# Optimization experiments

Measured on AMD Instinct MI355X. Metric: run time of the kernel, lower is better.

## Reference

```python
import jax, jax.numpy as jnp
import numpy as np

TOP_K = 32
OBS_RADIUS = 1.0
N = 4096
IN_DIM = 4


def setup_inputs() -> dict:
    key = jax.random.key(0)
    ks = jax.random.split(key, 10)
    s = 0.05
    return {
        "states": jax.random.normal(ks[0], (N, 4), jnp.float32),
        "goals": jax.random.normal(ks[1], (N, 2), jnp.float32),
        "W1": jax.random.normal(ks[2], (64, IN_DIM + 1), jnp.float32) * s,
        "b1": jnp.zeros((64,), jnp.float32),
        "W2": jax.random.normal(ks[3], (128, 64), jnp.float32) * s,
        "b2": jnp.zeros((128,), jnp.float32),
        "Wd1": jax.random.normal(ks[4], (64, 132), jnp.float32) * s,
        "bd1": jnp.zeros((64,), jnp.float32),
        "Wd2": jax.random.normal(ks[5], (128, 64), jnp.float32) * s,
        "bd2": jnp.zeros((128,), jnp.float32),
        "Wd3": jax.random.normal(ks[6], (64, 128), jnp.float32) * s,
        "bd3": jnp.zeros((64,), jnp.float32),
        "Wd4": jax.random.normal(ks[7], (4, 64), jnp.float32) * s,
        "bd4": jnp.zeros((4,), jnp.float32),
    }


def reference(states, goals, W1, b1, W2, b2, Wd1, bd1, Wd2, bd2, Wd3, bd3, Wd4, bd4):
    n = states.shape[0]
    dt = states.dtype
    # pairwise relative states + one-hot self indicator -> [N, N, 5]
    x = states[:, None, :] - states[None, :, :]
    x = jnp.concatenate([x, jnp.eye(n, dtype=dt)[:, :, None]], axis=2)
    # remove_distant_agents: keep TOP_K nearest neighbors by planar distance
    d = jnp.sqrt(jnp.sum(x[:, :, :2] ** 2, axis=2) + 1e-4)  # [N, N]
    _, idx = jax.lax.top_k(-d, TOP_K)                        # [N, K]
    xk = jnp.take_along_axis(x, idx[:, :, None], axis=1)     # [N, K, 5]
    # observation-radius mask (torch reshape [N,K,1]->[N,1,K] == transpose here)
    dist = jnp.linalg.norm(xk[:, :, :2], axis=2)             # [N, K]
    mask = (dist < OBS_RADIUS).astype(dt).reshape(n, 1, TOP_K)
    # NOTE: original uses a raw reshape [N,K,5]->[N,5,K] (not a transpose); match it
    h = xk.reshape(n, IN_DIM + 1, TOP_K)
    # pointwise (kernel-1) conv stack 5 -> 64 -> 128
    h = jax.nn.relu(jnp.einsum('oc,ncp->nop', W1, h) + b1[None, :, None])
    h = jax.nn.relu(jnp.einsum('oc,ncp->nop', W2, h) + b2[None, :, None])
    # original does torch.max(...)[1]: ARGMAX indices, promoted to float by cat
    x_local = jnp.argmax(h * mask, axis=2).astype(dt)        # [N, 128]
    rel = states[:, :2] - goals
    feat = jnp.concatenate([x_local, rel, states[:, 2:]], axis=1)  # [N, 132]
    z = jax.nn.relu(feat @ Wd1.T + bd1)
    z = jax.nn.relu(z @ Wd2.T + bd2)
    z = jax.nn.relu(z @ Wd3.T + bd3)
    z = z @ Wd4.T + bd4
    k = 2.0 * jax.nn.sigmoid(z) + 0.2                        # [N, 4] gains
    state = jnp.concatenate([rel, states[:, 2:]], axis=1)    # [N, 4]
    a_x = -(k[:, 0] * state[:, 0] + k[:, 1] * state[:, 2])
    a_y = -(k[:, 2] * state[:, 1] + k[:, 3] * state[:, 3])
    return jnp.stack([a_x, a_y], axis=1)                     # [N, 2]
```

## Files before the change

### kernel.cpp

```cpp
#include <hip/hip_runtime.h>
#include <math.h>

#define NAGENT 4096
#define TOPK 32
#define FAGB 8
#define CANDCAP 2048

__global__ __launch_bounds__(256) void topk_kernel(
    const float* __restrict__ states, int* __restrict__ idx_out)
{
    const int i = blockIdx.x;
    const int t = threadIdx.x;
    const int lane = t & 63;
    __shared__ unsigned int hist[1024];
    __shared__ unsigned int wsum[4];
    __shared__ unsigned long long cand[CANDCAP];
    __shared__ int ccount;
    __shared__ unsigned int cutB;

    #pragma unroll
    for (int u = 0; u < 4; ++u) hist[t + u * 256] = 0u;
    if (t == 0) ccount = 0;

    const float4 si = ((const float4*)states)[i];
    __syncthreads();

    unsigned int mybits[16];
    #pragma unroll
    for (int u = 0; u < 16; ++u) {
        int j = t + u * 256;
        float4 sj = ((const float4*)states)[j];
        float dx = __fsub_rn(si.x, sj.x);
        float dy = __fsub_rn(si.y, sj.y);
        float s  = __fadd_rn(__fadd_rn(__fmul_rn(dx, dx), __fmul_rn(dy, dy)), 1e-4f);
        float dv = sqrtf(s);
        mybits[u] = __float_as_uint(dv);
        unsigned int bin = (unsigned int)(dv * 256.0f);
        if (bin > 1023u) bin = 1023u;
        atomicAdd(&hist[bin], 1u);
    }
    __syncthreads();

    unsigned int h0 = hist[t * 4 + 0], h1 = hist[t * 4 + 1];
    unsigned int h2 = hist[t * 4 + 2], h3 = hist[t * 4 + 3];
    unsigned int v = h0 + h1 + h2 + h3;
    unsigned int inc = v;
    #pragma unroll
    for (int off = 1; off < 64; off <<= 1) {
        unsigned int u = __shfl_up(inc, off, 64);
        if (lane >= off) inc += u;
    }
    if (lane == 63) wsum[t >> 6] = inc;
    __syncthreads();
    unsigned int woff = 0;
    for (int w = 0; w < (t >> 6); ++w) woff += wsum[w];
    unsigned int incl = inc + woff;
    unsigned int exc  = incl - v;
    if (exc < TOPK && incl >= TOPK) {
        unsigned int cum = exc;
        unsigned int hh[4] = {h0, h1, h2, h3};
        int b = t * 4 + 3;
        #pragma unroll
        for (int q = 0; q < 4; ++q) {
            cum += hh[q];
            if (cum >= TOPK) { b = t * 4 + q; break; }
        }
        cutB = (unsigned int)b;
    }
    __syncthreads();

    const unsigned int B = cutB;
    #pragma unroll
    for (int u = 0; u < 16; ++u) {
        float dv = __uint_as_float(mybits[u]);
        unsigned int bin = (unsigned int)(dv * 256.0f);
        if (bin > 1023u) bin = 1023u;
        if (bin <= B) {
            int pos = atomicAdd(&ccount, 1);
            if (pos < CANDCAP)
                cand[pos] = ((unsigned long long)mybits[u] << 32)
                          | (unsigned int)(t + u * 256);
        }
    }
    __syncthreads();

    const int C = (ccount < CANDCAP) ? ccount : CANDCAP;
    for (int q = t; q < C; q += 256) {
        unsigned long long key = cand[q];
        int rank = 0;
        for (int r = 0; r < C; ++r) rank += (cand[r] < key) ? 1 : 0;
        if (rank < TOPK) idx_out[i * TOPK + rank] = (int)(key & 0xffffffffu);
    }
}

__global__ __launch_bounds__(256) void fused_kernel(
    const float* __restrict__ states, const float* __restrict__ goals,
    const float* __restrict__ W1,  const float* __restrict__ b1,
    const float* __restrict__ W2,  const float* __restrict__ b2,
    const float* __restrict__ Wd1, const float* __restrict__ bd1,
    const float* __restrict__ Wd2, const float* __restrict__ bd2,
    const float* __restrict__ Wd3, const float* __restrict__ bd3,
    const float* __restrict__ Wd4, const float* __restrict__ bd4,
    const int* __restrict__ idx_in, float* __restrict__ out)
{
    const int t = threadIdx.x;
    const int a = t >> 6;
    const int l = t & 63;
    const int base = blockIdx.x * FAGB;

    __shared__ __attribute__((aligned(16))) float w2a[64 * 68];
    __shared__ __attribute__((aligned(16))) float w2b[64 * 68];
    __shared__ __attribute__((aligned(16))) float w1s[320];
    __shared__ __attribute__((aligned(16))) float b1s[64];
    __shared__ __attribute__((aligned(16))) float b2s[128];
    __shared__ __attribute__((aligned(16))) float flat[4][160];
    __shared__ __attribute__((aligned(16))) float maskv[4][32];
    __shared__ __attribute__((aligned(16))) float featb[FAGB][132];
    __shared__ __attribute__((aligned(16))) float h1[4][2048];
    float* z1s = &h1[0][0];
    float* z2s = z1s + 512;
    float* z3s = z2s + 1024;
    float* kvs = z3s + 512;

    #pragma unroll
    for (int u = 0; u < 32; ++u) {
        int e = t + u * 256;
        int o = e >> 6, c = e & 63;
        float v = W2[e];
        int dst = c * 68 + ((o >> 3) << 2) + (o & 3);
        if (o & 4) w2b[dst] = v; else w2a[dst] = v;
    }
    for (int e = t; e < 320; e += 256) w1s[e] = W1[e];
    if (t < 64)  b1s[t] = b1[t];
    if (t < 128) b2s[t] = b2[t];
    __syncthreads();

    #pragma unroll
    for (int round = 0; round < 2; ++round) {
        const int g = round * 4 + a;
        const int i = base + g;

        if (l < 32) {
            int j = idx_in[i * TOPK + l];
            float4 sj  = ((const float4*)states)[j];
            float4 siv = ((const float4*)states)[i];
            float d0 = siv.x - sj.x;
            float d1 = siv.y - sj.y;
            float d2 = siv.z - sj.z;
            float d3 = siv.w - sj.w;
            flat[a][l * 5 + 0] = d0;
            flat[a][l * 5 + 1] = d1;
            flat[a][l * 5 + 2] = d2;
            flat[a][l * 5 + 3] = d3;
            flat[a][l * 5 + 4] = (j == i) ? 1.0f : 0.0f;
            float dist = sqrtf(__fadd_rn(__fmul_rn(d0, d0), __fmul_rn(d1, d1)));
            maskv[a][l] = (dist < 1.0f) ? 1.0f : 0.0f;
        } else if (l < 36) {
            int f = l - 32;
            float4 siv = ((const float4*)states)[i];
            float2 gi  = ((const float2*)goals)[i];
            float v = (f == 0) ? (siv.x - gi.x)
                    : (f == 1) ? (siv.y - gi.y)
                    : (f == 2) ? siv.z : siv.w;
            featb[g][128 + f] = v;
        }

        #pragma unroll
        for (int u = 0; u < 32; ++u) {
            int e = u * 64 + l;
            int p = e & 31, o1 = e >> 5;
            float acc = b1s[o1];
            #pragma unroll
            for (int f = 0; f < 5; ++f)
                acc += w1s[o1 * 5 + f] * flat[a][f * 32 + p];
            h1[a][o1 * 32 + p] = fmaxf(acc, 0.0f);
        }

        const int ow = l & 15;
        const int pt = l >> 4;
        float acc[8][8];
        #pragma unroll
        for (int k = 0; k < 8; ++k)
            #pragma unroll
            for (int q = 0; q < 8; ++q) acc[k][q] = 0.0f;

        for (int c4 = 0; c4 < 16; ++c4) {
            float4 wAv[4], wBv[4], hAv[4], hBv[4];
            #pragma unroll
            for (int cc = 0; cc < 4; ++cc) {
                int c = c4 * 4 + cc;
                wAv[cc] = *(const float4*)&w2a[c * 68 + ow * 4];
                wBv[cc] = *(const float4*)&w2b[c * 68 + ow * 4];
                hAv[cc] = *(const float4*)&h1[a][c * 32 + pt * 8];
                hBv[cc] = *(const float4*)&h1[a][c * 32 + pt * 8 + 4];
            }
            #pragma unroll
            for (int cc = 0; cc < 4; ++cc) {
                float wv[8] = {wAv[cc].x, wAv[cc].y, wAv[cc].z, wAv[cc].w,
                               wBv[cc].x, wBv[cc].y, wBv[cc].z, wBv[cc].w};
                float hv[8] = {hAv[cc].x, hAv[cc].y, hAv[cc].z, hAv[cc].w,
                               hBv[cc].x, hBv[cc].y, hBv[cc].z, hBv[cc].w};
                #pragma unroll
                for (int k = 0; k < 8; ++k)
                    #pragma unroll
                    for (int q = 0; q < 8; ++q)
                        acc[k][q] += wv[k] * hv[q];
            }
        }

        float4 mA = *(const float4*)&maskv[a][pt * 8];
        float4 mB = *(const float4*)&maskv[a][pt * 8 + 4];
        float mv[8] = {mA.x, mA.y, mA.z, mA.w, mB.x, mB.y, mB.z, mB.w};
        #pragma unroll
        for (int k = 0; k < 8; ++k) {
            float bb = b2s[ow * 8 + k];
            unsigned long long best = 0ull;
            #pragma unroll
            for (int q = 0; q < 8; ++q) {
                float val = fmaxf(acc[k][q] + bb, 0.0f) * mv[q];
                unsigned long long key =
                    ((unsigned long long)__float_as_uint(val) << 32)
                    | (unsigned int)(31 - (pt * 8 + q));
                if (key > best) best = key;
            }
            unsigned long long o1 = __shfl_xor(best, 16, 64); if (o1 > best) best = o1;
            unsigned long long o2 = __shfl_xor(best, 32, 64); if (o2 > best) best = o2;
            if (pt == 0) {
                int pbest = 31 - (int)(best & 63ull);
                featb[g][ow * 8 + k] = (float)pbest;
            }
        }
    }
    __syncthreads();

    const int g0 = 2 * a, g1 = 2 * a + 1;

    {
        float bb = bd1[l];
        float a0 = bb, a1 = bb;
        for (int k = 0; k < 33; ++k) {
            float4 wv = *(const float4*)&Wd1[l * 132 + 4 * k];
            float4 f0 = *(const float4*)&featb[g0][4 * k];
            float4 f1 = *(const float4*)&featb[g1][4 * k];
            a0 += wv.x * f0.x; a0 += wv.y * f0.y; a0 += wv.z * f0.z; a0 += wv.w * f0.w;
            a1 += wv.x * f1.x; a1 += wv.y * f1.y; a1 += wv.z * f1.z; a1 += wv.w * f1.w;
        }
        z1s[g0 * 64 + l] = fmaxf(a0, 0.0f);
        z1s[g1 * 64 + l] = fmaxf(a1, 0.0f);
    }

    {
        float accA0 = bd2[l], accA1 = bd2[l];
        float accB0 = bd2[l + 64], accB1 = bd2[l + 64];
        for (int k = 0; k < 16; ++k) {
            float4 wa = *(const float4*)&Wd2[l * 64 + 4 * k];
            float4 wb = *(const float4*)&Wd2[(l + 64) * 64 + 4 * k];
            float4 f0 = *(const float4*)&z1s[g0 * 64 + 4 * k];
            float4 f1 = *(const float4*)&z1s[g1 * 64 + 4 * k];
            accA0 += wa.x * f0.x; accA0 += wa.y * f0.y;
            accA0 += wa.z * f0.z; accA0 += wa.w * f0.w;
            accB0 += wb.x * f0.x; accB0 += wb.y * f0.y;
            accB0 += wb.z * f0.z; accB0 += wb.w * f0.w;
            accA1 += wa.x * f1.x; accA1 += wa.y * f1.y;
            accA1 += wa.z * f1.z; accA1 += wa.w * f1.w;
            accB1 += wb.x * f1.x; accB1 += wb.y * f1.y;
            accB1 += wb.z * f1.z; accB1 += wb.w * f1.w;
        }
        z2s[g0 * 128 + l]      = fmaxf(accA0, 0.0f);
        z2s[g0 * 128 + l + 64] = fmaxf(accB0, 0.0f);
        z2s[g1 * 128 + l]      = fmaxf(accA1, 0.0f);
        z2s[g1 * 128 + l + 64] = fmaxf(accB1, 0.0f);
    }

    {
        float bb = bd3[l];
        float a0 = bb, a1 = bb;
        for (int k = 0; k < 32; ++k) {
            float4 wv = *(const float4*)&Wd3[l * 128 + 4 * k];
            float4 f0 = *(const float4*)&z2s[g0 * 128 + 4 * k];
            float4 f1 = *(const float4*)&z2s[g1 * 128 + 4 * k];
            a0 += wv.x * f0.x; a0 += wv.y * f0.y; a0 += wv.z * f0.z; a0 += wv.w * f0.w;
            a1 += wv.x * f1.x; a1 += wv.y * f1.y; a1 += wv.z * f1.z; a1 += wv.w * f1.w;
        }
        z3s[g0 * 64 + l] = fmaxf(a0, 0.0f);
        z3s[g1 * 64 + l] = fmaxf(a1, 0.0f);
    }

    if (l < 8) {
        int gg = (l >> 2) ? g1 : g0;
        int o = l & 3;
        float acc = bd4[o];
        for (int c = 0; c < 64; ++c) acc += Wd4[o * 64 + c] * z3s[gg * 64 + c];
        kvs[gg * 4 + o] = 2.0f / (1.0f + expf(-acc)) + 0.2f;
    }
    if (l < 4) {
        int gg = (l >> 1) ? g1 : g0;
        int axis = l & 1;
        float ka = kvs[gg * 4 + 2 * axis + 0];
        float kb = kvs[gg * 4 + 2 * axis + 1];
        float rel = featb[gg][128 + axis];
        float vel = featb[gg][130 + axis];
        out[(base + gg) * 2 + axis] = -(ka * rel + kb * vel);
    }
}

extern "C" void kernel_launch(void* const* d_in, const int* in_sizes, int n_in,
                              void* d_out, int out_size, void* d_ws, size_t ws_size,
                              hipStream_t stream)
{
    const float* states = (const float*)d_in[0];
    const float* goals  = (const float*)d_in[1];
    const float* W1  = (const float*)d_in[2];
    const float* b1  = (const float*)d_in[3];
    const float* W2  = (const float*)d_in[4];
    const float* b2  = (const float*)d_in[5];
    const float* Wd1 = (const float*)d_in[6];
    const float* bd1 = (const float*)d_in[7];
    const float* Wd2 = (const float*)d_in[8];
    const float* bd2 = (const float*)d_in[9];
    const float* Wd3 = (const float*)d_in[10];
    const float* bd3 = (const float*)d_in[11];
    const float* Wd4 = (const float*)d_in[12];
    const float* bd4 = (const float*)d_in[13];

    int*   idx = (int*)d_ws;
    float* out = (float*)d_out;

    topk_kernel<<<NAGENT, 256, 0, stream>>>(states, idx);
    fused_kernel<<<NAGENT / FAGB, 256, 0, stream>>>(states, goals, W1, b1, W2, b2,
                                                    Wd1, bd1, Wd2, bd2, Wd3, bd3,
                                                    Wd4, bd4, idx, out);
}
```

Baseline: 140.4 us.

## Fuse top-k neighbor selection into main kernel with LDS-staged positions

Merges the separate top-k kernel into the fused MLP kernel. Each block first copies all agent xy positions into shared memory, then runs the histogram/candidate top-k for its 8 agents one after another, keeping indices in shared memory. A union shared buffer is reused later for W2 and the activations. This removes one launch and the global index round trip, but it drops the top-k grid from 4096 blocks to 512, serializes eight selections per block behind barriers, and the large shared-memory footprint limits occupancy.

```diff
diff --git a/kernel.cpp b/kernel.cpp
--- a/kernel.cpp
+++ b/kernel.cpp
@@ -6,94 +6,7 @@
 #define FAGB 8
 #define CANDCAP 2048
 
-__global__ __launch_bounds__(256) void topk_kernel(
-    const float* __restrict__ states, int* __restrict__ idx_out)
-{
-    const int i = blockIdx.x;
-    const int t = threadIdx.x;
-    const int lane = t & 63;
-    __shared__ unsigned int hist[1024];
-    __shared__ unsigned int wsum[4];
-    __shared__ unsigned long long cand[CANDCAP];
-    __shared__ int ccount;
-    __shared__ unsigned int cutB;
-
-    #pragma unroll
-    for (int u = 0; u < 4; ++u) hist[t + u * 256] = 0u;
-    if (t == 0) ccount = 0;
-
-    const float4 si = ((const float4*)states)[i];
-    __syncthreads();
-
-    unsigned int mybits[16];
-    #pragma unroll
-    for (int u = 0; u < 16; ++u) {
-        int j = t + u * 256;
-        float4 sj = ((const float4*)states)[j];
-        float dx = __fsub_rn(si.x, sj.x);
-        float dy = __fsub_rn(si.y, sj.y);
-        float s  = __fadd_rn(__fadd_rn(__fmul_rn(dx, dx), __fmul_rn(dy, dy)), 1e-4f);
-        float dv = sqrtf(s);
-        mybits[u] = __float_as_uint(dv);
-        unsigned int bin = (unsigned int)(dv * 256.0f);
-        if (bin > 1023u) bin = 1023u;
-        atomicAdd(&hist[bin], 1u);
-    }
-    __syncthreads();
-
-    unsigned int h0 = hist[t * 4 + 0], h1 = hist[t * 4 + 1];
-    unsigned int h2 = hist[t * 4 + 2], h3 = hist[t * 4 + 3];
-    unsigned int v = h0 + h1 + h2 + h3;
-    unsigned int inc = v;
-    #pragma unroll
-    for (int off = 1; off < 64; off <<= 1) {
-        unsigned int u = __shfl_up(inc, off, 64);
-        if (lane >= off) inc += u;
-    }
-    if (lane == 63) wsum[t >> 6] = inc;
-    __syncthreads();
-    unsigned int woff = 0;
-    for (int w = 0; w < (t >> 6); ++w) woff += wsum[w];
-    unsigned int incl = inc + woff;
-    unsigned int exc  = incl - v;
-    if (exc < TOPK && incl >= TOPK) {
-        unsigned int cum = exc;
-        unsigned int hh[4] = {h0, h1, h2, h3};
-        int b = t * 4 + 3;
-        #pragma unroll
-        for (int q = 0; q < 4; ++q) {
-            cum += hh[q];
-            if (cum >= TOPK) { b = t * 4 + q; break; }
-        }
-        cutB = (unsigned int)b;
-    }
-    __syncthreads();
-
-    const unsigned int B = cutB;
-    #pragma unroll
-    for (int u = 0; u < 16; ++u) {
-        float dv = __uint_as_float(mybits[u]);
-        unsigned int bin = (unsigned int)(dv * 256.0f);
-        if (bin > 1023u) bin = 1023u;
-        if (bin <= B) {
-            int pos = atomicAdd(&ccount, 1);
-            if (pos < CANDCAP)
-                cand[pos] = ((unsigned long long)mybits[u] << 32)
-                          | (unsigned int)(t + u * 256);
-        }
-    }
-    __syncthreads();
-
-    const int C = (ccount < CANDCAP) ? ccount : CANDCAP;
-    for (int q = t; q < C; q += 256) {
-        unsigned long long key = cand[q];
-        int rank = 0;
-        for (int r = 0; r < C; ++r) rank += (cand[r] < key) ? 1 : 0;
-        if (rank < TOPK) idx_out[i * TOPK + rank] = (int)(key & 0xffffffffu);
-    }
-}
-
-__global__ __launch_bounds__(256) void fused_kernel(
+__global__ __launch_bounds__(256) void fused_all_kernel(
     const float* __restrict__ states, const float* __restrict__ goals,
     const float* __restrict__ W1,  const float* __restrict__ b1,
     const float* __restrict__ W2,  const float* __restrict__ b2,
@@ -101,27 +14,117 @@
     const float* __restrict__ Wd2, const float* __restrict__ bd2,
     const float* __restrict__ Wd3, const float* __restrict__ bd3,
     const float* __restrict__ Wd4, const float* __restrict__ bd4,
-    const int* __restrict__ idx_in, float* __restrict__ out)
+    float* __restrict__ out)
 {
     const int t = threadIdx.x;
     const int a = t >> 6;
     const int l = t & 63;
     const int base = blockIdx.x * FAGB;
 
-    __shared__ __attribute__((aligned(16))) float w2a[64 * 68];
-    __shared__ __attribute__((aligned(16))) float w2b[64 * 68];
-    __shared__ __attribute__((aligned(16))) float w1s[320];
-    __shared__ __attribute__((aligned(16))) float b1s[64];
-    __shared__ __attribute__((aligned(16))) float b2s[128];
+    __shared__ __attribute__((aligned(16))) char uni[67584];
+    __shared__ int idxsel[FAGB][TOPK];
     __shared__ __attribute__((aligned(16))) float flat[4][160];
     __shared__ __attribute__((aligned(16))) float maskv[4][32];
     __shared__ __attribute__((aligned(16))) float featb[FAGB][132];
-    __shared__ __attribute__((aligned(16))) float h1[4][2048];
-    float* z1s = &h1[0][0];
-    float* z2s = z1s + 512;
-    float* z3s = z2s + 1024;
-    float* kvs = z3s + 512;
-
+    __shared__ __attribute__((aligned(16))) float w1s[320];
+    __shared__ unsigned int wsum[4];
+    __shared__ int ccount;
+    __shared__ unsigned int cutB;
+
+    float2* xy = (float2*)uni;
+    {
+        const float4* s4 = (const float4*)states;
+        #pragma unroll
+        for (int u = 0; u < 16; ++u) {
+            int e = t + u * 256;
+            float4 s = s4[e];
+            xy[e] = make_float2(s.x, s.y);
+        }
+    }
+    unsigned int* hist = (unsigned int*)(uni + 32768);
+    unsigned long long* cand = (unsigned long long*)(uni + 36864);
+    __syncthreads();
+
+    for (int g = 0; g < FAGB; ++g) {
+        const int i = base + g;
+        #pragma unroll
+        for (int u = 0; u < 4; ++u) hist[t + u * 256] = 0u;
+        if (t == 0) ccount = 0;
+        const float2 pi = xy[i];
+        __syncthreads();
+
+        unsigned int mybits[16];
+        #pragma unroll
+        for (int u = 0; u < 16; ++u) {
+            int j = t + u * 256;
+            float2 pj = xy[j];
+            float dx = __fsub_rn(pi.x, pj.x);
+            float dy = __fsub_rn(pi.y, pj.y);
+            float s  = __fadd_rn(__fadd_rn(__fmul_rn(dx, dx), __fmul_rn(dy, dy)), 1e-4f);
+            float dv = sqrtf(s);
+            mybits[u] = __float_as_uint(dv);
+            unsigned int bin = (unsigned int)(dv * 256.0f);
+            if (bin > 1023u) bin = 1023u;
+            atomicAdd(&hist[bin], 1u);
+        }
+        __syncthreads();
+
+        unsigned int h0 = hist[t * 4 + 0], h1v = hist[t * 4 + 1];
+        unsigned int h2v = hist[t * 4 + 2], h3v = hist[t * 4 + 3];
+        unsigned int v = h0 + h1v + h2v + h3v;
+        unsigned int inc = v;
+        #pragma unroll
+        for (int off = 1; off < 64; off <<= 1) {
+            unsigned int uu = __shfl_up(inc, off, 64);
+            if (l >= off) inc += uu;
+        }
+        if (l == 63) wsum[t >> 6] = inc;
+        __syncthreads();
+        unsigned int woff = 0;
+        for (int w = 0; w < (t >> 6); ++w) woff += wsum[w];
+        unsigned int incl = inc + woff;
+        unsigned int exc  = incl - v;
+        if (exc < TOPK && incl >= TOPK) {
+            unsigned int cum = exc;
+            unsigned int hh[4] = {h0, h1v, h2v, h3v};
+            int b = t * 4 + 3;
+            #pragma unroll
+            for (int q = 0; q < 4; ++q) {
+                cum += hh[q];
+                if (cum >= TOPK) { b = t * 4 + q; break; }
+            }
+            cutB = (unsigned int)b;
+        }
+        __syncthreads();
+
+        const unsigned int B = cutB;
+        #pragma unroll
+        for (int u = 0; u < 16; ++u) {
+            float dv = __uint_as_float(mybits[u]);
+            unsigned int bin = (unsigned int)(dv * 256.0f);
+            if (bin > 1023u) bin = 1023u;
+            if (bin <= B) {
+                int pos = atomicAdd(&ccount, 1);
+                if (pos < CANDCAP)
+                    cand[pos] = ((unsigned long long)mybits[u] << 32)
+                              | (unsigned int)(t + u * 256);
+            }
+        }
+        __syncthreads();
+
+        const int C = (ccount < CANDCAP) ? ccount : CANDCAP;
+        for (int q = t; q < C; q += 256) {
+            unsigned long long key = cand[q];
+            int rank = 0;
+            for (int r = 0; r < C; ++r) rank += (cand[r] < key) ? 1 : 0;
+            if (rank < TOPK) idxsel[g][rank] = (int)(key & 0xffffffffu);
+        }
+        __syncthreads();
+    }
+
+    float* w2a = (float*)uni;
+    float* w2b = (float*)(uni + 17408);
+    float* h1p = (float*)(uni + 34816);
     #pragma unroll
     for (int u = 0; u < 32; ++u) {
         int e = t + u * 256;
@@ -131,8 +134,6 @@
         if (o & 4) w2b[dst] = v; else w2a[dst] = v;
     }
     for (int e = t; e < 320; e += 256) w1s[e] = W1[e];
-    if (t < 64)  b1s[t] = b1[t];
-    if (t < 128) b2s[t] = b2[t];
     __syncthreads();
 
     #pragma unroll
@@ -141,7 +142,7 @@
         const int i = base + g;
 
         if (l < 32) {
-            int j = idx_in[i * TOPK + l];
+            int j = idxsel[g][l];
             float4 sj  = ((const float4*)states)[j];
             float4 siv = ((const float4*)states)[i];
             float d0 = siv.x - sj.x;
@@ -169,11 +170,11 @@
         for (int u = 0; u < 32; ++u) {
             int e = u * 64 + l;
             int p = e & 31, o1 = e >> 5;
-            float acc = b1s[o1];
+            float acc = b1[o1];
             #pragma unroll
             for (int f = 0; f < 5; ++f)
                 acc += w1s[o1 * 5 + f] * flat[a][f * 32 + p];
-            h1[a][o1 * 32 + p] = fmaxf(acc, 0.0f);
+            h1p[a * 2048 + o1 * 32 + p] = fmaxf(acc, 0.0f);
         }
 
         const int ow = l & 15;
@@ -191,8 +192,8 @@
                 int c = c4 * 4 + cc;
                 wAv[cc] = *(const float4*)&w2a[c * 68 + ow * 4];
                 wBv[cc] = *(const float4*)&w2b[c * 68 + ow * 4];
-                hAv[cc] = *(const float4*)&h1[a][c * 32 + pt * 8];
-                hBv[cc] = *(const float4*)&h1[a][c * 32 + pt * 8 + 4];
+                hAv[cc] = *(const float4*)&h1p[a * 2048 + c * 32 + pt * 8];
+                hBv[cc] = *(const float4*)&h1p[a * 2048 + c * 32 + pt * 8 + 4];
             }
             #pragma unroll
             for (int cc = 0; cc < 4; ++cc) {
@@ -213,7 +214,7 @@
         float mv[8] = {mA.x, mA.y, mA.z, mA.w, mB.x, mB.y, mB.z, mB.w};
         #pragma unroll
         for (int k = 0; k < 8; ++k) {
-            float bb = b2s[ow * 8 + k];
+            float bb = b2[ow * 8 + k];
             unsigned long long best = 0ull;
             #pragma unroll
             for (int q = 0; q < 8; ++q) {
@@ -233,6 +234,10 @@
     }
     __syncthreads();
 
+    float* z1s = h1p;
+    float* z2s = z1s + 512;
+    float* z3s = z2s + 1024;
+    float* kvs = z3s + 512;
     const int g0 = 2 * a, g1 = 2 * a + 1;
 
     {
@@ -323,11 +328,9 @@
     const float* Wd4 = (const float*)d_in[12];
     const float* bd4 = (const float*)d_in[13];
 
-    int*   idx = (int*)d_ws;
     float* out = (float*)d_out;
 
-    topk_kernel<<<NAGENT, 256, 0, stream>>>(states, idx);
-    fused_kernel<<<NAGENT / FAGB, 256, 0, stream>>>(states, goals, W1, b1, W2, b2,
-                                                    Wd1, bd1, Wd2, bd2, Wd3, bd3,
-                                                    Wd4, bd4, idx, out);
+    fused_all_kernel<<<NAGENT / FAGB, 256, 0, stream>>>(states, goals, W1, b1,
+                                                        W2, b2, Wd1, bd1, Wd2, bd2,
+                                                        Wd3, bd3, Wd4, bd4, out);
 }
```

Measured after the change: 219.6 us. 56.4% more time.
